# Performance work log

Measured on AMD Instinct MI355X. Metric: run time of the kernel, lower is better.

## Reference

```python
import jax, jax.numpy as jnp
import numpy as np
from math import sqrt

N_HEADS = 16

def _rope(t, freqs):
    # t: [b, n, l, hd]; freqs: [l, hd//2, 2] (real, imag of unit rotations)
    b, n, l, hd = t.shape
    t2 = t.reshape(b, n, l, hd // 2, 2)
    tr, ti = t2[..., 0], t2[..., 1]
    fr, fi = freqs[..., 0], freqs[..., 1]  # broadcast over b, n
    out_r = tr * fr - ti * fi
    out_i = tr * fi + ti * fr
    return jnp.stack([out_r, out_i], axis=-1).reshape(b, n, l, hd)

def setup_inputs() -> dict:
    key = jax.random.key(0)
    ks = jax.random.split(key, 6)
    B, L, D = 2, 2048, 1024
    HD = D // N_HEADS
    x = jax.random.normal(ks[0], (B, L, D), dtype=jnp.float32)
    # proper rotary frequencies: theta_i = 10000^{-2i/hd}, angle = pos * theta
    inv = 1.0 / (10000.0 ** (np.arange(0, HD, 2, dtype=np.float32) / HD))  # [HD//2]
    ang = np.arange(L, dtype=np.float32)[:, None] * inv[None, :]           # [L, HD//2]
    freqs = jnp.asarray(np.stack([np.cos(ang), np.sin(ang)], axis=-1))     # [L, HD//2, 2]
    # additive causal mask
    causal = jnp.tril(jnp.ones((L, L), dtype=bool))
    attention_mask = jnp.where(causal, 0.0, -1e9).astype(jnp.float32)[None, None]
    init = 1.0 / sqrt(D)
    Wq = jax.random.normal(ks[1], (D, D), dtype=jnp.float32) * init
    Wk = jax.random.normal(ks[2], (D, D), dtype=jnp.float32) * init
    Wv = jax.random.normal(ks[3], (D, D), dtype=jnp.float32) * init
    Wo = jax.random.normal(ks[4], (D, D), dtype=jnp.float32) * init
    return {"x": x, "freqs": freqs, "attention_mask": attention_mask,
            "Wq": Wq, "Wk": Wk, "Wv": Wv, "Wo": Wo}

def reference(x, freqs, attention_mask, Wq, Wk, Wv, Wo):
    b, l, d = x.shape
    n = N_HEADS
    hd = d // n
    scale = sqrt(hd)

    def split_heads(t):  # [b, l, d] -> [b, n, l, hd]
        return t.reshape(b, l, n, hd).transpose(0, 2, 1, 3)

    q = split_heads(x @ Wq.T)
    k = split_heads(x @ Wk.T)
    v = split_heads(x @ Wv.T)
    q = _rope(q, freqs)
    k = _rope(k, freqs)
    scores = jnp.einsum('bnqd,bnkd->bnqk', q, k) / scale
    attn = jax.nn.softmax(scores + attention_mask, axis=-1)
    out = jnp.einsum('bnqk,bnkd->bnqd', attn, v)
    out = out.transpose(0, 2, 1, 3).reshape(b, l, d)
    return out @ Wo.T
```

## Files before the change

kernel.cpp:

```cpp
#include <hip/hip_runtime.h>
#include <stdint.h>

#define LSEQ 2048
#define DMODEL 1024
#define NHEADS 16
#define HDIM 64
#define MROWS 4096

typedef __attribute__((ext_vector_type(8))) short short8;
typedef __attribute__((ext_vector_type(4))) float f32x4;
typedef __attribute__((ext_vector_type(16))) float f32x16;

static __device__ __forceinline__ unsigned short f2bf(float f) {
    unsigned u = __builtin_bit_cast(unsigned, f);
    u += 0x7fffu + ((u >> 16) & 1u);
    return (unsigned short)(u >> 16);
}
static __device__ __forceinline__ unsigned cvt_pk_bf16(float a, float b) {
    unsigned r;
    asm("v_cvt_pk_bf16_f32 %0, %1, %2" : "=v"(r) : "v"(a), "v"(b));
    return r;
}

static __device__ __forceinline__ void gl2lds16(const unsigned short* g, unsigned short* l) {
    __builtin_amdgcn_global_load_lds(
        (const __attribute__((address_space(1))) unsigned int*)g,
        (__attribute__((address_space(3))) unsigned int*)l, 16, 0, 0);
}

__global__ void cast_all(const float* __restrict__ x,  const float* __restrict__ Wq,
                         const float* __restrict__ Wk, const float* __restrict__ Wv,
                         const float* __restrict__ Wo,
                         unsigned short* __restrict__ xb,
                         unsigned short* __restrict__ wqkv,
                         unsigned short* __restrict__ wo) {
    int i = blockIdx.x * blockDim.x + threadIdx.x;
    const float4* src;
    ushort4* dst;
    if (i < 1048576) {
        src = (const float4*)x + i;
        dst = (ushort4*)xb + i;
    } else {
        int t = i - 1048576;
        int w = t >> 18;
        int j = t & 262143;
        const float* s = (w == 0) ? Wq : (w == 1) ? Wk : (w == 2) ? Wv : Wo;
        src = (const float4*)s + j;
        dst = (w == 3) ? ((ushort4*)wo + j) : ((ushort4*)wqkv + (size_t)w * 262144 + j);
    }
    float4 v = *src;
    ushort4 o;
    o.x = f2bf(v.x); o.y = f2bf(v.y); o.z = f2bf(v.z); o.w = f2bf(v.w);
    *dst = o;
}

template <int TM, bool OUT_BF16>
__global__ __launch_bounds__(256) void gemm_nt(const unsigned short* __restrict__ A,
                                               const unsigned short* __restrict__ Bw,
                                               void* __restrict__ C,
                                               int Kdim, int ldc) {
    constexpr int WM = TM / 2;
    __shared__ unsigned short As[TM * 32];
    __shared__ unsigned short Bs[128 * 32];
    int tid = threadIdx.x;
    int lane = tid & 63, wave = tid >> 6;
    int row16 = lane & 15, quad = lane >> 4;
    int wm = wave & 1, wn = wave >> 1;
    int m0 = blockIdx.x * TM;
    int n0 = blockIdx.y * 128;

    int srow = wave * 16 + (lane >> 2);
    int scol = (lane & 3) * 8;
    const unsigned short* Ag = A  + (size_t)(m0 + srow) * Kdim + scol;
    const unsigned short* Bg = Bw + (size_t)(n0 + srow) * Kdim + scol;
    unsigned short* Asw = As + wave * 512;
    unsigned short* Bsw = Bs + wave * 512;

    f32x4 acc[WM / 16][4];
    #pragma unroll
    for (int i = 0; i < WM / 16; ++i)
        #pragma unroll
        for (int j = 0; j < 4; ++j) acc[i][j] = (f32x4){0.f, 0.f, 0.f, 0.f};

    for (int k0 = 0; k0 < Kdim; k0 += 32) {
        #pragma unroll
        for (int i = 0; i < TM / 64; ++i)
            gl2lds16(Ag + (size_t)i * 64 * Kdim + k0, Asw + i * 2048);
        gl2lds16(Bg + k0, Bsw);
        gl2lds16(Bg + (size_t)64 * Kdim + k0, Bsw + 2048);
        __syncthreads();

        short8 af[WM / 16], bf_[4];
        #pragma unroll
        for (int mi = 0; mi < WM / 16; ++mi)
            af[mi] = *(const short8*)(As + (wm * WM + mi * 16 + row16) * 32 + quad * 8);
        #pragma unroll
        for (int ni = 0; ni < 4; ++ni)
            bf_[ni] = *(const short8*)(Bs + (wn * 64 + ni * 16 + row16) * 32 + quad * 8);
        #pragma unroll
        for (int mi = 0; mi < WM / 16; ++mi)
            #pragma unroll
            for (int ni = 0; ni < 4; ++ni)
                acc[mi][ni] = __builtin_amdgcn_mfma_f32_16x16x32_bf16(af[mi], bf_[ni], acc[mi][ni], 0, 0, 0);
        __syncthreads();
    }

    int orow = m0 + wm * WM + quad * 4;
    int ocol = n0 + wn * 64 + row16;
    #pragma unroll
    for (int mi = 0; mi < WM / 16; ++mi)
        #pragma unroll
        for (int ni = 0; ni < 4; ++ni)
            #pragma unroll
            for (int r = 0; r < 4; ++r) {
                size_t idx = (size_t)(orow + mi * 16 + r) * ldc + (ocol + ni * 16);
                if (OUT_BF16) ((unsigned short*)C)[idx] = f2bf(acc[mi][ni][r]);
                else          ((float*)C)[idx]          = acc[mi][ni][r];
            }
}


#define VM_NOP
#define VM_W4 asm volatile("s_waitcnt vmcnt(4)" ::: "memory");
#define VM_W0 asm volatile("s_waitcnt vmcnt(0)" ::: "memory");

#define QKV_PH(KK, MH, DO_STAGE, LDST, GSRC, VMW)                            \
  {                                                                          \
    if ((MH) == 0) {                                                         \
      const unsigned short* Bp = lds + rs + 16384 + (KK) * 8192 + boff;      \
      _Pragma("unroll")                                                      \
      for (int j = 0; j < 4; ++j) bfr[j] = *(const short8*)(Bp + j * 512);   \
    }                                                                        \
    short8 af[4];                                                            \
    {                                                                        \
      const unsigned short* Ap = lds + rs + (KK) * 8192 + aoff + (MH) * 2048;\
      _Pragma("unroll")                                                      \
      for (int i = 0; i < 4; ++i) af[i] = *(const short8*)(Ap + i * 512);    \
    }                                                                        \
    if (DO_STAGE) {                                                          \
      const unsigned short* gp = (GSRC);                                     \
      gl2lds16(gp,          lds + (LDST) + wave * 512);                      \
      gl2lds16(gp + 131072, lds + (LDST) + 4096 + wave * 512);               \
    }                                                                        \
    VMW                                                                      \
    __builtin_amdgcn_sched_barrier(0);                                       \
    __builtin_amdgcn_s_barrier();                                            \
    __builtin_amdgcn_sched_barrier(0);                                       \
    __builtin_amdgcn_s_setprio(1);                                           \
    _Pragma("unroll")                                                        \
    for (int i = 0; i < 4; ++i)                                              \
      _Pragma("unroll")                                                      \
      for (int j = 0; j < 4; ++j)                                            \
        acc[(MH) * 4 + i][j] = __builtin_amdgcn_mfma_f32_16x16x32_bf16(      \
            af[i], bfr[j], acc[(MH) * 4 + i][j], 0, 0, 0);                   \
    __builtin_amdgcn_s_setprio(0);                                           \
    __builtin_amdgcn_s_barrier();                                            \
  }

__global__ __launch_bounds__(512, 2) void gemm_qkv(const unsigned short* __restrict__ A,
                                                   const unsigned short* __restrict__ Bw,
                                                   const float* __restrict__ freqs,
                                                   unsigned short* __restrict__ qh,
                                                   unsigned short* __restrict__ kh,
                                                   unsigned short* __restrict__ vt) {
    extern __shared__ unsigned short lds[];

    int tid  = threadIdx.x;
    int lane = tid & 63, wave = tid >> 6;
    int row16 = lane & 15, quad = lane >> 4;
    int wm = wave & 1, wn = wave >> 1;

    int id  = blockIdx.x;
    int gid = (id & 7) * 24 + (id >> 3);
    int bx = gid / 12, by = gid % 12;
    int m0 = bx * 256, n0 = by * 256;

    int off0 = tid * 16;
    int g = off0 ^ (((off0 >> 7) & 3) << 4);
    int srow = g >> 6;
    int scol = (g & 63) >> 1;
    const unsigned short* AgL = A  + (size_t)(m0 + srow) * DMODEL + scol;
    const unsigned short* BgL = Bw + (size_t)(n0 + srow) * DMODEL + scol;

    int sw   = ((row16 >> 1) & 3) << 4;
    int aoff = (wm * 128 + row16) * 32 + (((quad * 16) ^ sw) >> 1);
    int boff = (wn *  64 + row16) * 32 + (((quad * 16) ^ sw) >> 1);

    f32x4 acc[8][4];
    #pragma unroll
    for (int i = 0; i < 8; ++i)
        #pragma unroll
        for (int j = 0; j < 4; ++j) acc[i][j] = (f32x4){0.f, 0.f, 0.f, 0.f};

    gl2lds16(AgL,                lds + 0     + wave * 512);
    gl2lds16(AgL + 131072,       lds + 4096  + wave * 512);
    gl2lds16(BgL,                lds + 16384 + wave * 512);
    gl2lds16(BgL + 131072,       lds + 20480 + wave * 512);
    gl2lds16(AgL + 32,           lds + 8192  + wave * 512);
    gl2lds16(AgL + 32 + 131072,  lds + 12288 + wave * 512);
    gl2lds16(BgL + 32,           lds + 24576 + wave * 512);
    gl2lds16(BgL + 32 + 131072,  lds + 28672 + wave * 512);
    asm volatile("s_waitcnt vmcnt(4)" ::: "memory");
    __builtin_amdgcn_s_barrier();

    short8 bfr[4];
    for (int t = 0; t < 15; ++t) {
        const int rs = (t & 1) * 32768;
        const int ws = ((t + 1) & 1) * 32768;
        const unsigned short* An = AgL + (t + 1) * 64;
        const unsigned short* Bn = BgL + (t + 1) * 64;
        QKV_PH(0, 0, true, ws + 0,     An,      VM_NOP)
        QKV_PH(0, 1, true, ws + 16384, Bn,      VM_W4)
        QKV_PH(1, 0, true, ws + 8192,  An + 32, VM_NOP)
        QKV_PH(1, 1, true, ws + 24576, Bn + 32, VM_W4)
    }
    {
        const int rs = 32768;
        QKV_PH(0, 0, false, 0, AgL, VM_NOP)
        QKV_PH(0, 1, false, 0, AgL, VM_W0)
        QKV_PH(1, 0, false, 0, AgL, VM_NOP)
        QKV_PH(1, 1, false, 0, AgL, VM_NOP)
    }

    int region = n0 >> 10;
    int b = m0 >> 11;
    int orow0 = m0 + wm * 128 + quad * 4;
    int ocol0 = n0 + wn * 64 + row16;

    if (region < 2) {
        unsigned short* dst = region ? kh : qh;
        float sgn = (row16 & 1) ? 1.f : -1.f;
        #pragma unroll
        for (int nf = 0; nf < 4; ++nf) {
            int c = ocol0 - region * 1024 + nf * 16;
            int head = c >> 6, d = c & 63, ii = d >> 1;
            unsigned short* hb = dst + ((size_t)(b * NHEADS + head) * LSEQ) * HDIM + d;
            #pragma unroll
            for (int mf = 0; mf < 8; ++mf)
                #pragma unroll
                for (int r = 0; r < 4; ++r) {
                    int l = (orow0 + mf * 16 + r) & 2047;
                    float own = acc[mf][nf][r];
                    float par = __shfl_xor(own, 1);
                    float2 f = *(const float2*)(freqs + ((size_t)l * 32 + ii) * 2);
                    float out = own * f.x + par * (sgn * f.y);
                    hb[(size_t)l * HDIM] = f2bf(out);
                }
        }
    } else {
        #pragma unroll
        for (int nf = 0; nf < 4; ++nf) {
            int c = ocol0 - 2048 + nf * 16;
            int head = c >> 6, d = c & 63;
            size_t vbase = ((size_t)(b * NHEADS + head) * HDIM + d) * LSEQ;
            #pragma unroll
            for (int mf = 0; mf < 8; ++mf) {
                int l0 = (orow0 + mf * 16) & 2047;
                ushort4 o;
                o.x = f2bf(acc[mf][nf][0]);
                o.y = f2bf(acc[mf][nf][1]);
                o.z = f2bf(acc[mf][nf][2]);
                o.w = f2bf(acc[mf][nf][3]);
                *(ushort4*)(vt + vbase + l0) = o;
            }
        }
    }
}

__global__ __launch_bounds__(256, 4) void attn_flash(const unsigned short* __restrict__ qh,
                                                     const unsigned short* __restrict__ kh,
                                                     const unsigned short* __restrict__ vt,
                                                     unsigned short* __restrict__ oh) {
    __shared__ char smem[33280];
    unsigned short* ldsb = (unsigned short*)smem;
    float* mO = (float*)smem;
    float* mL = (float*)(smem + 16384);
    const float CS = 0.18033688011112042f;
    const float CB = 28.853900817779268f;

    int lane = threadIdx.x & 63;
    int wave = threadIdx.x >> 6;
    int l31 = lane & 31;
    int h   = lane >> 5;
    int kq  = wave >> 1, qq = wave & 1;

    int id  = blockIdx.x;
    int xcd = id & 7;
    int bn  = xcd * 4 + ((id >> 3) & 3);
    int s   = id >> 5;
    int u = s & 7, rnd = s >> 3;
    int qb = (rnd == 0) ? (31 - u) : (rnd == 1) ? (16 + u) : (rnd == 2) ? (15 - u) : u;
    int b = bn >> 4, n = bn & 15;

    const unsigned short* Qb = qh + (size_t)bn * LSEQ * HDIM;
    const unsigned short* Kb = kh + (size_t)bn * LSEQ * HDIM;
    const unsigned short* Vb = vt + (size_t)bn * HDIM * LSEQ;

    int q0 = qb * 64;
    int qabs = q0 + qq * 32 + l31;

    short8 qf[4];
    #pragma unroll
    for (int mf = 0; mf < 4; ++mf)
        qf[mf] = *(const short8*)(Qb + (size_t)(q0 + qq * 32 + l31) * HDIM + mf * 16 + h * 8);

    int sf  = wave >> 1;
    int m0s = (wave & 1) * 2;
    const unsigned short* kg = Kb + (size_t)(sf * 32 + l31) * HDIM + m0s * 16 + h * 8;
    const unsigned short* vg = Vb + (size_t)(sf * 32 + l31) * LSEQ + m0s * 16 + h * 8;
    int soff = (sf * 4 + m0s) * 512;

    f32x16 accO[2];
    #pragma unroll
    for (int i = 0; i < 16; ++i) { accO[0][i] = 0.f; accO[1][i] = 0.f; }
    float l_s = 0.f;

    int nk = qb + 1;

    auto stage = [&](int t) {
        int sl = (t & 1) * 4096;
        const unsigned short* kgk = kg + (size_t)t * 64 * HDIM;
        const unsigned short* vgk = vg + t * 64;
        gl2lds16(kgk,      ldsb + sl + soff);
        gl2lds16(kgk + 16, ldsb + sl + soff + 512);
        gl2lds16(vgk,      ldsb + 8192 + sl + soff);
        gl2lds16(vgk + 16, ldsb + 8192 + sl + soff + 512);
    };

    stage(0);
    stage(1);

    for (int kt = 0; kt < nk; ++kt) {
        if (kt < nk - 1) asm volatile("s_waitcnt vmcnt(4)" ::: "memory");
        else             asm volatile("s_waitcnt vmcnt(0)" ::: "memory");
        __builtin_amdgcn_s_barrier();
        __builtin_amdgcn_sched_barrier(0);

        int cb = (kt & 1) * 4096;
        const unsigned short* Kc = ldsb + cb;
        const unsigned short* Vc = ldsb + 8192 + cb;

        bool edge = (kt == nk - 1);
        bool dead = edge && (kq == 1) && (qq == 0);

        if (!dead) {
            f32x16 z;
            #pragma unroll
            for (int i = 0; i < 16; ++i) z[i] = 0.f;
            __builtin_amdgcn_s_setprio(1);
            #pragma unroll
            for (int m = 0; m < 4; ++m) {
                short8 kf = *(const short8*)(Kc + (kq * 4 + m) * 512 + lane * 8);
                z = __builtin_amdgcn_mfma_f32_32x32x16_bf16(kf, qf[m], z, 0, 0, 0);
            }
            __builtin_amdgcn_s_setprio(0);

            float p[16];
            bool maskz = edge && (kq == qq);
            #pragma unroll
            for (int r = 0; r < 16; ++r) {
                float e = __builtin_amdgcn_exp2f(z[r] * CS - CB);
                if (maskz) {
                    int kabs = kt * 64 + kq * 32 + (r & 3) + 8 * (r >> 2) + 4 * h;
                    if (kabs > qabs) e = 0.f;
                }
                p[r] = e;
            }
            float ps = 0.f;
            #pragma unroll
            for (int r = 0; r < 16; ++r) ps += p[r];
            l_s += ps;

            uint2 P4[4];
            #pragma unroll
            for (int g = 0; g < 4; ++g) {
                P4[g].x = cvt_pk_bf16(p[4 * g],     p[4 * g + 1]);
                P4[g].y = cvt_pk_bf16(p[4 * g + 2], p[4 * g + 3]);
            }
            short8 bfr[2];
            bool hb = (h != 0);
            #pragma unroll
            for (int m = 0; m < 2; ++m) {
                uint2 own = hb ? P4[1 + 2 * m] : P4[2 * m];
                uint2 snd = hb ? P4[2 * m]     : P4[1 + 2 * m];
                uint2 rcv;
                rcv.x = __shfl_xor(snd.x, 32);
                rcv.y = __shfl_xor(snd.y, 32);
                uint4 bb;
                bb.x = hb ? rcv.x : own.x;
                bb.y = hb ? rcv.y : own.y;
                bb.z = hb ? own.x : rcv.x;
                bb.w = hb ? own.y : rcv.y;
                bfr[m] = __builtin_bit_cast(short8, bb);
            }

            __builtin_amdgcn_s_setprio(1);
            #pragma unroll
            for (int dq = 0; dq < 2; ++dq)
                #pragma unroll
                for (int m = 0; m < 2; ++m) {
                    short8 vf = *(const short8*)(Vc + (dq * 4 + kq * 2 + m) * 512 + lane * 8);
                    accO[dq] = __builtin_amdgcn_mfma_f32_32x32x16_bf16(vf, bfr[m], accO[dq], 0, 0, 0);
                }
            __builtin_amdgcn_s_setprio(0);
        }

        __builtin_amdgcn_sched_barrier(0);
        __builtin_amdgcn_s_barrier();
        if (kt + 2 < nk) stage(kt + 2);
    }

    l_s += __shfl_xor(l_s, 32);

    if (kq == 1) {
        #pragma unroll
        for (int dq = 0; dq < 2; ++dq)
            #pragma unroll
            for (int r = 0; r < 16; ++r)
                mO[(qq * 2 + dq) * 1024 + r * 64 + lane] = accO[dq][r];
        mL[qq * 64 + lane] = l_s;
    }
    __syncthreads();
    if (kq == 0) {
        float inv = 1.0f / (l_s + mL[qq * 64 + lane]);
        #pragma unroll
        for (int dq = 0; dq < 2; ++dq)
            #pragma unroll
            for (int g = 0; g < 4; ++g) {
                float o0 = (accO[dq][4 * g]     + mO[(qq * 2 + dq) * 1024 + (4 * g)     * 64 + lane]) * inv;
                float o1 = (accO[dq][4 * g + 1] + mO[(qq * 2 + dq) * 1024 + (4 * g + 1) * 64 + lane]) * inv;
                float o2 = (accO[dq][4 * g + 2] + mO[(qq * 2 + dq) * 1024 + (4 * g + 2) * 64 + lane]) * inv;
                float o3 = (accO[dq][4 * g + 3] + mO[(qq * 2 + dq) * 1024 + (4 * g + 3) * 64 + lane]) * inv;
                ushort4 o;
                o.x = f2bf(o0); o.y = f2bf(o1); o.z = f2bf(o2); o.w = f2bf(o3);
                int d = dq * 32 + 8 * g + 4 * h;
                *(ushort4*)(oh + (size_t)(b * LSEQ + q0 + qq * 32 + l31) * DMODEL + n * HDIM + d) = o;
            }
    }
}

extern "C" void kernel_launch(void* const* d_in, const int* in_sizes, int n_in,
                              void* d_out, int out_size, void* d_ws, size_t ws_size,
                              hipStream_t stream) {
    const float* x     = (const float*)d_in[0];
    const float* freqs = (const float*)d_in[1];
    const float* Wq = (const float*)d_in[3];
    const float* Wk = (const float*)d_in[4];
    const float* Wv = (const float*)d_in[5];
    const float* Wo = (const float*)d_in[6];

    char* ws = (char*)d_ws;
    unsigned short* xb   = (unsigned short*)ws; ws += (size_t)MROWS * DMODEL * 2;
    unsigned short* wqkv = (unsigned short*)ws; ws += (size_t)3 * DMODEL * DMODEL * 2;
    unsigned short* wo   = (unsigned short*)ws; ws += (size_t)DMODEL * DMODEL * 2;
    unsigned short* qh   = (unsigned short*)ws; ws += (size_t)32 * LSEQ * HDIM * 2;
    unsigned short* kh   = (unsigned short*)ws; ws += (size_t)32 * LSEQ * HDIM * 2;
    unsigned short* vt   = (unsigned short*)ws; ws += (size_t)32 * HDIM * LSEQ * 2;
    unsigned short* oh   = (unsigned short*)ws; ws += (size_t)MROWS * DMODEL * 2;

    static bool attr_set = false;
    if (!attr_set) {
        (void)hipFuncSetAttribute((const void*)gemm_qkv,
                                  hipFuncAttributeMaxDynamicSharedMemorySize, 131072);
        attr_set = true;
    }

    cast_all<<<8192, 256, 0, stream>>>(x, Wq, Wk, Wv, Wo, xb, wqkv, wo);

    gemm_qkv<<<192, 512, 131072, stream>>>(xb, wqkv, freqs, qh, kh, vt);

    attn_flash<<<1024, 256, 0, stream>>>(qh, kh, vt, oh);

    gemm_nt<64, false><<<dim3(MROWS / 64, DMODEL / 128), 256, 0, stream>>>(oh, wo, (float*)d_out, DMODEL, DMODEL);
}
```

Before: 197.8 us.

## Prefetch QKV GEMM fragments one phase ahead; pair causal query blocks per attention CTA

The QKV GEMM now double-buffers its A and B register fragments, so the LDS reads for the next phase are issued right after the barrier and overlap the current MFMAs instead of sitting ahead of them. The attention kernel launches half as many blocks, and each block processes two query blocks (31-p and p) so every CTA gets the same causal workload. The aim is to hide LDS latency in the GEMM and remove tail imbalance in attention. In exchange, the GEMM uses more registers and the attention kernel has less parallelism and adds an extra sync between its two query blocks.

Result: no change. 198.8 us (+0.5%).

```diff
diff --git a/kernel.cpp b/kernel.cpp
--- a/kernel.cpp
+++ b/kernel.cpp
@@ -124,37 +124,46 @@
 #define VM_W4 asm volatile("s_waitcnt vmcnt(4)" ::: "memory");
 #define VM_W0 asm volatile("s_waitcnt vmcnt(0)" ::: "memory");
 
-#define QKV_PH(KK, MH, DO_STAGE, LDST, GSRC, VMW)                            \
-  {                                                                          \
-    if ((MH) == 0) {                                                         \
-      const unsigned short* Bp = lds + rs + 16384 + (KK) * 8192 + boff;      \
-      _Pragma("unroll")                                                      \
-      for (int j = 0; j < 4; ++j) bfr[j] = *(const short8*)(Bp + j * 512);   \
-    }                                                                        \
-    short8 af[4];                                                            \
-    {                                                                        \
-      const unsigned short* Ap = lds + rs + (KK) * 8192 + aoff + (MH) * 2048;\
-      _Pragma("unroll")                                                      \
-      for (int i = 0; i < 4; ++i) af[i] = *(const short8*)(Ap + i * 512);    \
-    }                                                                        \
-    if (DO_STAGE) {                                                          \
-      const unsigned short* gp = (GSRC);                                     \
-      gl2lds16(gp,          lds + (LDST) + wave * 512);                      \
-      gl2lds16(gp + 131072, lds + (LDST) + 4096 + wave * 512);               \
-    }                                                                        \
-    VMW                                                                      \
-    __builtin_amdgcn_sched_barrier(0);                                       \
-    __builtin_amdgcn_s_barrier();                                            \
-    __builtin_amdgcn_sched_barrier(0);                                       \
-    __builtin_amdgcn_s_setprio(1);                                           \
-    _Pragma("unroll")                                                        \
-    for (int i = 0; i < 4; ++i)                                              \
-      _Pragma("unroll")                                                      \
-      for (int j = 0; j < 4; ++j)                                            \
-        acc[(MH) * 4 + i][j] = __builtin_amdgcn_mfma_f32_16x16x32_bf16(      \
-            af[i], bfr[j], acc[(MH) * 4 + i][j], 0, 0, 0);                   \
-    __builtin_amdgcn_s_setprio(0);                                           \
-    __builtin_amdgcn_s_barrier();                                            \
+#define QKV_PH(S, T, DO_STAGE, DO_AHEAD, VMW)                                 \
+  {                                                                           \
+    if (DO_STAGE) {                                                           \
+      int ws = (((T) + 1) & 1) * 32768;                                       \
+      const unsigned short* gp = ((S) & 1)                                    \
+          ? (BgL + ((size_t)((T) + 1)) * 64 + ((S) >> 1) * 32)                \
+          : (AgL + ((size_t)((T) + 1)) * 64 + ((S) >> 1) * 32);               \
+      int ldst = ws + (((S) & 1) ? 16384 : 0) + ((S) >> 1) * 8192;            \
+      gl2lds16(gp,          lds + ldst + wave * 512);                         \
+      gl2lds16(gp + 131072, lds + ldst + 4096 + wave * 512);                  \
+    }                                                                         \
+    VMW                                                                       \
+    __builtin_amdgcn_sched_barrier(0);                                        \
+    __builtin_amdgcn_s_barrier();                                             \
+    __builtin_amdgcn_sched_barrier(0);                                        \
+    if (DO_AHEAD) {                                                           \
+      const int sn = ((S) + 1) & 3;                                           \
+      const int tn = ((S) == 3) ? (T) + 1 : (T);                              \
+      const int rsn = (tn & 1) * 32768;                                       \
+      if (sn == 0 || sn == 2) {                                               \
+        const unsigned short* Bp = lds + rsn + 16384 + (sn >> 1) * 8192 + boff; \
+        _Pragma("unroll")                                                     \
+        for (int j = 0; j < 4; ++j)                                           \
+          bfr[(sn >> 1) & 1][j] = *(const short8*)(Bp + j * 512);             \
+      }                                                                       \
+      const unsigned short* Ap = lds + rsn + (sn >> 1) * 8192 + aoff + (sn & 1) * 2048; \
+      _Pragma("unroll")                                                       \
+      for (int i = 0; i < 4; ++i)                                             \
+        af[sn & 1][i] = *(const short8*)(Ap + i * 512);                       \
+    }                                                                         \
+    __builtin_amdgcn_sched_barrier(0);                                        \
+    __builtin_amdgcn_s_setprio(1);                                            \
+    _Pragma("unroll")                                                         \
+    for (int i = 0; i < 4; ++i)                                               \
+      _Pragma("unroll")                                                       \
+      for (int j = 0; j < 4; ++j)                                             \
+        acc[((S) & 1) * 4 + i][j] = __builtin_amdgcn_mfma_f32_16x16x32_bf16(  \
+            af[(S) & 1][i], bfr[((S) >> 1) & 1][j], acc[((S) & 1) * 4 + i][j], 0, 0, 0); \
+    __builtin_amdgcn_s_setprio(0);                                            \
+    __builtin_amdgcn_s_barrier();                                             \
   }
 
 __global__ __launch_bounds__(512, 2) void gemm_qkv(const unsigned short* __restrict__ A,
@@ -203,24 +212,26 @@
     asm volatile("s_waitcnt vmcnt(4)" ::: "memory");
     __builtin_amdgcn_s_barrier();
 
-    short8 bfr[4];
+    short8 af[2][4], bfr[2][4];
+    {
+        const unsigned short* Bp = lds + 16384 + boff;
+        #pragma unroll
+        for (int j = 0; j < 4; ++j) bfr[0][j] = *(const short8*)(Bp + j * 512);
+        const unsigned short* Ap = lds + aoff;
+        #pragma unroll
+        for (int i = 0; i < 4; ++i) af[0][i] = *(const short8*)(Ap + i * 512);
+    }
+
     for (int t = 0; t < 15; ++t) {
-        const int rs = (t & 1) * 32768;
-        const int ws = ((t + 1) & 1) * 32768;
-        const unsigned short* An = AgL + (t + 1) * 64;
-        const unsigned short* Bn = BgL + (t + 1) * 64;
-        QKV_PH(0, 0, true, ws + 0,     An,      VM_NOP)
-        QKV_PH(0, 1, true, ws + 16384, Bn,      VM_W4)
-        QKV_PH(1, 0, true, ws + 8192,  An + 32, VM_NOP)
-        QKV_PH(1, 1, true, ws + 24576, Bn + 32, VM_W4)
-    }
-    {
-        const int rs = 32768;
-        QKV_PH(0, 0, false, 0, AgL, VM_NOP)
-        QKV_PH(0, 1, false, 0, AgL, VM_W0)
-        QKV_PH(1, 0, false, 0, AgL, VM_NOP)
-        QKV_PH(1, 1, false, 0, AgL, VM_NOP)
-    }
+        QKV_PH(0, t, true, true, VM_NOP)
+        QKV_PH(1, t, true, true, VM_W4)
+        QKV_PH(2, t, true, true, VM_NOP)
+        QKV_PH(3, t, true, true, VM_W4)
+    }
+    QKV_PH(0, 15, false, true,  VM_NOP)
+    QKV_PH(1, 15, false, true,  VM_W0)
+    QKV_PH(2, 15, false, true,  VM_NOP)
+    QKV_PH(3, 15, false, false, VM_NOP)
 
     int region = n0 >> 10;
     int b = m0 >> 11;
@@ -287,35 +298,18 @@
     int id  = blockIdx.x;
     int xcd = id & 7;
     int bn  = xcd * 4 + ((id >> 3) & 3);
-    int s   = id >> 5;
-    int u = s & 7, rnd = s >> 3;
-    int qb = (rnd == 0) ? (31 - u) : (rnd == 1) ? (16 + u) : (rnd == 2) ? (15 - u) : u;
+    int p   = id >> 5;
     int b = bn >> 4, n = bn & 15;
 
     const unsigned short* Qb = qh + (size_t)bn * LSEQ * HDIM;
     const unsigned short* Kb = kh + (size_t)bn * LSEQ * HDIM;
     const unsigned short* Vb = vt + (size_t)bn * HDIM * LSEQ;
-
-    int q0 = qb * 64;
-    int qabs = q0 + qq * 32 + l31;
-
-    short8 qf[4];
-    #pragma unroll
-    for (int mf = 0; mf < 4; ++mf)
-        qf[mf] = *(const short8*)(Qb + (size_t)(q0 + qq * 32 + l31) * HDIM + mf * 16 + h * 8);
 
     int sf  = wave >> 1;
     int m0s = (wave & 1) * 2;
     const unsigned short* kg = Kb + (size_t)(sf * 32 + l31) * HDIM + m0s * 16 + h * 8;
     const unsigned short* vg = Vb + (size_t)(sf * 32 + l31) * LSEQ + m0s * 16 + h * 8;
     int soff = (sf * 4 + m0s) * 512;
-
-    f32x16 accO[2];
-    #pragma unroll
-    for (int i = 0; i < 16; ++i) { accO[0][i] = 0.f; accO[1][i] = 0.f; }
-    float l_s = 0.f;
-
-    int nk = qb + 1;
 
     auto stage = [&](int t) {
         int sl = (t & 1) * 4096;
@@ -327,116 +321,137 @@
         gl2lds16(vgk + 16, ldsb + 8192 + sl + soff + 512);
     };
 
-    stage(0);
-    stage(1);
-
-    for (int kt = 0; kt < nk; ++kt) {
-        if (kt < nk - 1) asm volatile("s_waitcnt vmcnt(4)" ::: "memory");
-        else             asm volatile("s_waitcnt vmcnt(0)" ::: "memory");
-        __builtin_amdgcn_s_barrier();
-        __builtin_amdgcn_sched_barrier(0);
-
-        int cb = (kt & 1) * 4096;
-        const unsigned short* Kc = ldsb + cb;
-        const unsigned short* Vc = ldsb + 8192 + cb;
-
-        bool edge = (kt == nk - 1);
-        bool dead = edge && (kq == 1) && (qq == 0);
-
-        if (!dead) {
-            f32x16 z;
-            #pragma unroll
-            for (int i = 0; i < 16; ++i) z[i] = 0.f;
-            __builtin_amdgcn_s_setprio(1);
-            #pragma unroll
-            for (int m = 0; m < 4; ++m) {
-                short8 kf = *(const short8*)(Kc + (kq * 4 + m) * 512 + lane * 8);
-                z = __builtin_amdgcn_mfma_f32_32x32x16_bf16(kf, qf[m], z, 0, 0, 0);
+    auto run_qb = [&](int qb) {
+        int q0 = qb * 64;
+        int qabs = q0 + qq * 32 + l31;
+
+        short8 qf[4];
+        #pragma unroll
+        for (int mf = 0; mf < 4; ++mf)
+            qf[mf] = *(const short8*)(Qb + (size_t)(q0 + qq * 32 + l31) * HDIM + mf * 16 + h * 8);
+
+        f32x16 accO[2];
+        #pragma unroll
+        for (int i = 0; i < 16; ++i) { accO[0][i] = 0.f; accO[1][i] = 0.f; }
+        float l_s = 0.f;
+
+        int nk = qb + 1;
+
+        stage(0);
+        stage(1);
+
+        for (int kt = 0; kt < nk; ++kt) {
+            if (kt < nk - 1) asm volatile("s_waitcnt vmcnt(4)" ::: "memory");
+            else             asm volatile("s_waitcnt vmcnt(0)" ::: "memory");
+            __builtin_amdgcn_s_barrier();
+            __builtin_amdgcn_sched_barrier(0);
+
+            int cb = (kt & 1) * 4096;
+            const unsigned short* Kc = ldsb + cb;
+            const unsigned short* Vc = ldsb + 8192 + cb;
+
+            bool edge = (kt == nk - 1);
+            bool dead = edge && (kq == 1) && (qq == 0);
+
+            if (!dead) {
+                f32x16 z;
+                #pragma unroll
+                for (int i = 0; i < 16; ++i) z[i] = 0.f;
+                __builtin_amdgcn_s_setprio(1);
+                #pragma unroll
+                for (int m = 0; m < 4; ++m) {
+                    short8 kf = *(const short8*)(Kc + (kq * 4 + m) * 512 + lane * 8);
+                    z = __builtin_amdgcn_mfma_f32_32x32x16_bf16(kf, qf[m], z, 0, 0, 0);
+                }
+                __builtin_amdgcn_s_setprio(0);
+
+                float p_[16];
+                bool maskz = edge && (kq == qq);
+                #pragma unroll
+                for (int r = 0; r < 16; ++r) {
+                    float e = __builtin_amdgcn_exp2f(z[r] * CS - CB);
+                    if (maskz) {
+                        int kabs = kt * 64 + kq * 32 + (r & 3) + 8 * (r >> 2) + 4 * h;
+                        if (kabs > qabs) e = 0.f;
+                    }
+                    p_[r] = e;
+                }
+                float ps = 0.f;
+                #pragma unroll
+                for (int r = 0; r < 16; ++r) ps += p_[r];
+                l_s += ps;
+
+                uint2 P4[4];
+                #pragma unroll
+                for (int g = 0; g < 4; ++g) {
+                    P4[g].x = cvt_pk_bf16(p_[4 * g],     p_[4 * g + 1]);
+                    P4[g].y = cvt_pk_bf16(p_[4 * g + 2], p_[4 * g + 3]);
+                }
+                short8 bfr[2];
+                bool hb = (h != 0);
+                #pragma unroll
+                for (int m = 0; m < 2; ++m) {
+                    uint2 own = hb ? P4[1 + 2 * m] : P4[2 * m];
+                    uint2 snd = hb ? P4[2 * m]     : P4[1 + 2 * m];
+                    uint2 rcv;
+                    rcv.x = __shfl_xor(snd.x, 32);
+                    rcv.y = __shfl_xor(snd.y, 32);
+                    uint4 bb;
+                    bb.x = hb ? rcv.x : own.x;
+                    bb.y = hb ? rcv.y : own.y;
+                    bb.z = hb ? own.x : rcv.x;
+                    bb.w = hb ? own.y : rcv.y;
+                    bfr[m] = __builtin_bit_cast(short8, bb);
+                }
+
+                __builtin_amdgcn_s_setprio(1);
+                #pragma unroll
+                for (int dq = 0; dq < 2; ++dq)
+                    #pragma unroll
+                    for (int m = 0; m < 2; ++m) {
+                        short8 vf = *(const short8*)(Vc + (dq * 4 + kq * 2 + m) * 512 + lane * 8);
+                        accO[dq] = __builtin_amdgcn_mfma_f32_32x32x16_bf16(vf, bfr[m], accO[dq], 0, 0, 0);
+                    }
+                __builtin_amdgcn_s_setprio(0);
             }
-            __builtin_amdgcn_s_setprio(0);
-
-            float p[16];
-            bool maskz = edge && (kq == qq);
-            #pragma unroll
-            for (int r = 0; r < 16; ++r) {
-                float e = __builtin_amdgcn_exp2f(z[r] * CS - CB);
-                if (maskz) {
-                    int kabs = kt * 64 + kq * 32 + (r & 3) + 8 * (r >> 2) + 4 * h;
-                    if (kabs > qabs) e = 0.f;
-                }
-                p[r] = e;
-            }
-            float ps = 0.f;
-            #pragma unroll
-            for (int r = 0; r < 16; ++r) ps += p[r];
-            l_s += ps;
-
-            uint2 P4[4];
-            #pragma unroll
-            for (int g = 0; g < 4; ++g) {
-                P4[g].x = cvt_pk_bf16(p[4 * g],     p[4 * g + 1]);
-                P4[g].y = cvt_pk_bf16(p[4 * g + 2], p[4 * g + 3]);
-            }
-            short8 bfr[2];
-            bool hb = (h != 0);
-            #pragma unroll
-            for (int m = 0; m < 2; ++m) {
-                uint2 own = hb ? P4[1 + 2 * m] : P4[2 * m];
-                uint2 snd = hb ? P4[2 * m]     : P4[1 + 2 * m];
-                uint2 rcv;
-                rcv.x = __shfl_xor(snd.x, 32);
-                rcv.y = __shfl_xor(snd.y, 32);
-                uint4 bb;
-                bb.x = hb ? rcv.x : own.x;
-                bb.y = hb ? rcv.y : own.y;
-                bb.z = hb ? own.x : rcv.x;
-                bb.w = hb ? own.y : rcv.y;
-                bfr[m] = __builtin_bit_cast(short8, bb);
-            }
-
-            __builtin_amdgcn_s_setprio(1);
+
+            __builtin_amdgcn_sched_barrier(0);
+            __builtin_amdgcn_s_barrier();
+            if (kt + 2 < nk) stage(kt + 2);
+        }
+
+        l_s += __shfl_xor(l_s, 32);
+
+        if (kq == 1) {
             #pragma unroll
             for (int dq = 0; dq < 2; ++dq)
                 #pragma unroll
-                for (int m = 0; m < 2; ++m) {
-                    short8 vf = *(const short8*)(Vc + (dq * 4 + kq * 2 + m) * 512 + lane * 8);
-                    accO[dq] = __builtin_amdgcn_mfma_f32_32x32x16_bf16(vf, bfr[m], accO[dq], 0, 0, 0);
-                }
-            __builtin_amdgcn_s_setprio(0);
+                for (int r = 0; r < 16; ++r)
+                    mO[(qq * 2 + dq) * 1024 + r * 64 + lane] = accO[dq][r];
+            mL[qq * 64 + lane] = l_s;
         }
-
-        __builtin_amdgcn_sched_barrier(0);
-        __builtin_amdgcn_s_barrier();
-        if (kt + 2 < nk) stage(kt + 2);
-    }
-
-    l_s += __shfl_xor(l_s, 32);
-
-    if (kq == 1) {
-        #pragma unroll
-        for (int dq = 0; dq < 2; ++dq)
-            #pragma unroll
-            for (int r = 0; r < 16; ++r)
-                mO[(qq * 2 + dq) * 1024 + r * 64 + lane] = accO[dq][r];
-        mL[qq * 64 + lane] = l_s;
-    }
-    __syncthreads();
-    if (kq == 0) {
-        float inv = 1.0f / (l_s + mL[qq * 64 + lane]);
-        #pragma unroll
-        for (int dq = 0; dq < 2; ++dq)
-            #pragma unroll
-            for (int g = 0; g < 4; ++g) {
-                float o0 = (accO[dq][4 * g]     + mO[(qq * 2 + dq) * 1024 + (4 * g)     * 64 + lane]) * inv;
-                float o1 = (accO[dq][4 * g + 1] + mO[(qq * 2 + dq) * 1024 + (4 * g + 1) * 64 + lane]) * inv;
-                float o2 = (accO[dq][4 * g + 2] + mO[(qq * 2 + dq) * 1024 + (4 * g + 2) * 64 + lane]) * inv;
-                float o3 = (accO[dq][4 * g + 3] + mO[(qq * 2 + dq) * 1024 + (4 * g + 3) * 64 + lane]) * inv;
-                ushort4 o;
-                o.x = f2bf(o0); o.y = f2bf(o1); o.z = f2bf(o2); o.w = f2bf(o3);
-                int d = dq * 32 + 8 * g + 4 * h;
-                *(ushort4*)(oh + (size_t)(b * LSEQ + q0 + qq * 32 + l31) * DMODEL + n * HDIM + d) = o;
-            }
-    }
+        __syncthreads();
+        if (kq == 0) {
+            float inv = 1.0f / (l_s + mL[qq * 64 + lane]);
+            #pragma unroll
+            for (int dq = 0; dq < 2; ++dq)
+                #pragma unroll
+                for (int g = 0; g < 4; ++g) {
+                    float o0 = (accO[dq][4 * g]     + mO[(qq * 2 + dq) * 1024 + (4 * g)     * 64 + lane]) * inv;
+                    float o1 = (accO[dq][4 * g + 1] + mO[(qq * 2 + dq) * 1024 + (4 * g + 1) * 64 + lane]) * inv;
+                    float o2 = (accO[dq][4 * g + 2] + mO[(qq * 2 + dq) * 1024 + (4 * g + 2) * 64 + lane]) * inv;
+                    float o3 = (accO[dq][4 * g + 3] + mO[(qq * 2 + dq) * 1024 + (4 * g + 3) * 64 + lane]) * inv;
+                    ushort4 o;
+                    o.x = f2bf(o0); o.y = f2bf(o1); o.z = f2bf(o2); o.w = f2bf(o3);
+                    int d = dq * 32 + 8 * g + 4 * h;
+                    *(ushort4*)(oh + (size_t)(b * LSEQ + q0 + qq * 32 + l31) * DMODEL + n * HDIM + d) = o;
+                }
+        }
+        __syncthreads();
+    };
+
+    run_qb(31 - p);
+    run_qb(p);
 }
 
 extern "C" void kernel_launch(void* const* d_in, const int* in_sizes, int n_in,
@@ -469,7 +484,7 @@
 
     gemm_qkv<<<192, 512, 131072, stream>>>(xb, wqkv, freqs, qh, kh, vt);
 
-    attn_flash<<<1024, 256, 0, stream>>>(qh, kh, vt, oh);
+    attn_flash<<<512, 256, 0, stream>>>(qh, kh, vt, oh);
 
     gemm_nt<64, false><<<dim3(MROWS / 64, DMODEL / 128), 256, 0, stream>>>(oh, wo, (float*)d_out, DMODEL, DMODEL);
 }
```
